# Performance work log

Hardware: AMD Instinct MI355X
Metric: run time of the kernel (lower is better)

The kernel has to match this reference:

```python
import jax, jax.numpy as jnp
import numpy as np

HEADS = 8
EPS = 1e-5

def setup_inputs() -> dict:
    key = jax.random.key(0)
    ks = jax.random.split(key, 4)
    B, S, N, C = 1, 256, 384, 512
    msa = jax.random.normal(ks[0], (B, S, N, C), dtype=jnp.float32)
    mask = jnp.ones((B, S), dtype=jnp.int32)
    Wqkv = jax.random.normal(ks[1], (3 * C, C), dtype=jnp.float32) * (C ** -0.5)
    bqkv = jnp.zeros((3 * C,), dtype=jnp.float32)
    Wout = jax.random.normal(ks[2], (C, C), dtype=jnp.float32) * (C ** -0.5)
    bout = jnp.zeros((C,), dtype=jnp.float32)
    gamma = jnp.ones((C,), dtype=jnp.float32)
    beta = jnp.zeros((C,), dtype=jnp.float32)
    return {"msa": msa, "mask": mask, "Wqkv": Wqkv, "bqkv": bqkv,
            "Wout": Wout, "bout": bout, "gamma": gamma, "beta": beta}

def reference(msa, mask, Wqkv, bqkv, Wout, bout, gamma, beta):
    B, S, N, C = msa.shape
    H = HEADS
    Dh = C // H
    scale = Dh ** -0.5
    msa_t = jnp.transpose(msa, (0, 2, 1, 3))            # [B,N,S,C]
    qkv = msa_t @ Wqkv.T + bqkv                          # [B,N,S,3C]
    qkv = qkv.reshape(B, N, S, 3, H, Dh)
    q, k, v = qkv[..., 0, :, :], qkv[..., 1, :, :], qkv[..., 2, :, :]  # [B,N,S,H,Dh]
    attn = jnp.einsum('bnshc,bnthc->bhst', q, k) * scale  # reduce over N and head-dim
    attn = jnp.where(mask[:, None, None, :] == 0, -1e9, attn)
    attn = jax.nn.softmax(attn, axis=-1)                 # [B,H,S,S]
    out = jnp.einsum('bhst,bnthc->bnshc', attn, v).reshape(B, N, S, C)
    out = jnp.transpose(out, (0, 2, 1, 3))               # [B,S,N,C]
    out = out @ Wout.T + bout
    x = msa + out
    mu = jnp.mean(x, axis=-1, keepdims=True)
    var = jnp.mean((x - mu) ** 2, axis=-1, keepdims=True)
    return (x - mu) * jax.lax.rsqrt(var + EPS) * gamma + beta
```

## Files before the change

### kernel.cpp

```cpp
#include <hip/hip_runtime.h>

#define S_ 256
#define N_ 384
#define C_ 512
#define H_ 8
#define R_ (N_*S_)
#define SPLITK 32
#define NPK (N_/SPLITK)

typedef _Float16 f16;
typedef _Float16 f16x8 __attribute__((ext_vector_type(8)));
typedef float f32x4 __attribute__((ext_vector_type(4)));

#define MFMA16(a,b,c) __builtin_amdgcn_mfma_f32_16x16x32_f16(a,b,c,0,0,0)

typedef __attribute__((address_space(3))) unsigned int as3_u32;
typedef __attribute__((address_space(1))) const unsigned int as1_u32;

__device__ __forceinline__ void gl_lds16(const void* g, void* l) {
    __builtin_amdgcn_global_load_lds((as1_u32*)(unsigned long long)g,
                                     (as3_u32*)(unsigned long long)l, 16, 0, 0);
}

__device__ __forceinline__ int swz_off(int row, int g) {
    return row*64 + (((g) ^ (row & 7)) << 3);
}

__device__ __forceinline__ void stage8(const f16* __restrict__ Ab,
                                       const f16* __restrict__ Bb,
                                       int stride, f16* As_, f16* Bs_,
                                       int tid, int wid) {
#pragma unroll
    for (int i = 0; i < 2; ++i) {
        int id = (i << 9) + tid;
        int row = id >> 3, g = (id & 7) ^ (row & 7);
        int lofs = ((i << 9) + (wid << 6)) << 4;
        gl_lds16(Ab + row * stride + (g << 3), (char*)As_ + lofs);
        gl_lds16(Bb + row * stride + (g << 3), (char*)Bs_ + lofs);
    }
}

__device__ __forceinline__ void mma8(const f16* As_, const f16* Bs_,
                                     int lane, int wr, int wc, f32x4 acc[4][2]) {
#pragma unroll
    for (int ks = 0; ks < 64; ks += 32) {
        int kg = (ks >> 3) + (lane >> 4);
        f16x8 af[4], bf[2];
#pragma unroll
        for (int m = 0; m < 4; ++m)
            af[m] = *(const f16x8*)&As_[swz_off(wr + (m << 4) + (lane & 15), kg)];
#pragma unroll
        for (int j = 0; j < 2; ++j)
            bf[j] = *(const f16x8*)&Bs_[swz_off(wc + (j << 4) + (lane & 15), kg)];
#pragma unroll
        for (int m = 0; m < 4; ++m)
#pragma unroll
            for (int j = 0; j < 2; ++j)
                acc[m][j] = MFMA16(af[m], bf[j], acc[m][j]);
    }
}

__device__ __forceinline__ void frag_mma64(const f16* As_, const f16* Bs_,
                                           int lane, int wr, int wc, f32x4 acc[4][4]) {
#pragma unroll
    for (int ks = 0; ks < 64; ks += 32) {
        int kg = (ks >> 3) + (lane >> 4);
        f16x8 af[4], bf[4];
#pragma unroll
        for (int m = 0; m < 4; ++m)
            af[m] = *(const f16x8*)&As_[swz_off(wr + (m << 4) + (lane & 15), kg)];
#pragma unroll
        for (int j = 0; j < 4; ++j)
            bf[j] = *(const f16x8*)&Bs_[swz_off(wc + (j << 4) + (lane & 15), kg)];
#pragma unroll
        for (int m = 0; m < 4; ++m)
#pragma unroll
            for (int j = 0; j < 4; ++j)
                acc[m][j] = MFMA16(af[m], bf[j], acc[m][j]);
    }
}

__global__ __launch_bounds__(256) void k_prep(const float* __restrict__ Wqkv,
                                              const float* __restrict__ Wout,
                                              f16* __restrict__ Wq16, f16* __restrict__ Wo16) {
    int i = blockIdx.x * 256 + threadIdx.x;
    if (i < 1536 * C_) Wq16[i] = (f16)Wqkv[i];
    if (i < C_ * C_)   Wo16[i] = (f16)Wout[i];
}

__global__ __launch_bounds__(256) void k_cast(const float* __restrict__ msa,
                                              f16* __restrict__ msaT) {
    int t = blockIdx.x * 256 + threadIdx.x;
    int r = t >> 6, cg = t & 63;
    int n = r >> 8, s = r & 255;
    const float* src = msa + (s * N_ + n) * C_ + (cg << 3);
    float4 lo = *(const float4*)src;
    float4 hi = *(const float4*)(src + 4);
    f16x8 v;
    v[0]=(f16)lo.x; v[1]=(f16)lo.y; v[2]=(f16)lo.z; v[3]=(f16)lo.w;
    v[4]=(f16)hi.x; v[5]=(f16)hi.y; v[6]=(f16)hi.z; v[7]=(f16)hi.w;
    *(f16x8*)(msaT + r * C_ + (cg << 3)) = v;
}

__global__ __launch_bounds__(512) void k_qkv(const f16* __restrict__ msaT,
                                             const f16* __restrict__ W,
                                             const float* __restrict__ bqkv,
                                             f16* __restrict__ qk,
                                             f16* __restrict__ vT) {
    int wg = (blockIdx.x & 7) * 1152 + (blockIdx.x >> 3);
    int bx = wg / 12, by = wg % 12;
    int j0 = by << 7;
    int tid = threadIdx.x, lane = tid & 63, wid = tid >> 6;
    int wr = (wid >> 2) << 6, wc = (wid & 3) << 5;
    __shared__ f16 SH[32768];
    const f16* Abase = msaT + (bx << 7) * C_;
    const f16* Bbase = W + j0 * C_;
    f32x4 acc[4][2] = {};
    stage8(Abase, Bbase, C_, SH, SH + 8192, tid, wid);
    __syncthreads();
    for (int kt = 0; kt < 8; ++kt) {
        int cur = kt & 1;
        if (kt < 7)
            stage8(Abase + ((kt + 1) << 6), Bbase + ((kt + 1) << 6), C_,
                   SH + ((cur ^ 1) << 14), SH + 8192 + ((cur ^ 1) << 14), tid, wid);
        mma8(SH + (cur << 14), SH + 8192 + (cur << 14), lane, wr, wc, acc);
        __syncthreads();
    }
    if (by < 8) {
#pragma unroll
        for (int m = 0; m < 4; ++m) {
            int rl = wr + (m << 4) + ((lane >> 4) << 2);
#pragma unroll
            for (int j = 0; j < 2; ++j) {
                int col = wc + (j << 4) + (lane & 15);
                float bv = bqkv[j0 + col];
#pragma unroll
                for (int q = 0; q < 4; ++q)
                    SH[(rl + q) * 140 + col] = (f16)(acc[m][j][q] + bv);
            }
        }
        __syncthreads();
#pragma unroll
        for (int i = 0; i < 4; ++i) {
            int u = (i << 9) + tid;
            int row = u >> 4, seg = u & 15;
            *(f16x8*)(qk + ((bx << 7) + row) * 1024 + j0 + (seg << 3)) =
                *(const f16x8*)&SH[row * 140 + (seg << 3)];
        }
    } else {
        int n = bx >> 1, t0g = (bx & 1) << 7;
#pragma unroll
        for (int m = 0; m < 4; ++m) {
            int rl = wr + (m << 4) + ((lane >> 4) << 2);
#pragma unroll
            for (int j = 0; j < 2; ++j) {
                int col = wc + (j << 4) + (lane & 15);
                float bv = bqkv[1024 + ((by - 8) << 7) + col];
#pragma unroll
                for (int q = 0; q < 4; ++q)
                    SH[col * 140 + rl + q] = (f16)(acc[m][j][q] + bv);
            }
        }
        __syncthreads();
#pragma unroll
        for (int i = 0; i < 4; ++i) {
            int u = (i << 9) + tid;
            int lcol = u >> 4, seg = u & 15;
            int jg = ((by - 8) << 7) + lcol;
            *(f16x8*)(vT + ((n * H_ + (jg >> 6)) * 64 + (jg & 63)) * S_ + t0g + (seg << 3)) =
                *(const f16x8*)&SH[lcol * 140 + (seg << 3)];
        }
    }
}

__global__ __launch_bounds__(512) void k_logits(const f16* __restrict__ qk,
                                                float* __restrict__ logP) {
    int wg = (blockIdx.x & 7) * 128 + (blockIdx.x >> 3);
    int sk = wg >> 5, rem = wg & 31, h = rem >> 2, sb = (rem >> 1) & 1, tb = rem & 1;
    int s0 = sb << 7, t0 = tb << 7, n0 = sk * NPK;
    int tid = threadIdx.x, lane = tid & 63, wid = tid >> 6;
    int wr = (wid >> 2) << 6, wc = (wid & 3) << 5;
    __shared__ f16 SH[32768];
    const f16* Aroot = qk + s0 * 1024 + (h << 6);
    const f16* Broot = qk + t0 * 1024 + 512 + (h << 6);
    f32x4 acc[4][2] = {};
    stage8(Aroot + n0 * S_ * 1024, Broot + n0 * S_ * 1024, 1024,
           SH, SH + 8192, tid, wid);
    __syncthreads();
    for (int t = 0; t < NPK; ++t) {
        int cur = t & 1;
        if (t < NPK - 1) {
            int n = n0 + t + 1;
            stage8(Aroot + n * S_ * 1024, Broot + n * S_ * 1024, 1024,
                   SH + ((cur ^ 1) << 14), SH + 8192 + ((cur ^ 1) << 14), tid, wid);
        }
        mma8(SH + (cur << 14), SH + 8192 + (cur << 14), lane, wr, wc, acc);
        __syncthreads();
    }
#pragma unroll
    for (int m = 0; m < 4; ++m) {
        int rl = wr + (m << 4) + ((lane >> 4) << 2);
#pragma unroll
        for (int j = 0; j < 2; ++j) {
            int tc = t0 + wc + (j << 4) + (lane & 15);
#pragma unroll
            for (int q = 0; q < 4; ++q)
                logP[((sk * H_ + h) * S_ + s0 + rl + q) * S_ + tc] = acc[m][j][q];
        }
    }
}

__global__ __launch_bounds__(256) void k_softmax(const float* __restrict__ logP,
                                                 const int* __restrict__ mask,
                                                 f16* __restrict__ attn) {
    int hs = blockIdx.x;
    int t = threadIdx.x, lane = t & 63, wid = t >> 6;
    float v = 0.f;
#pragma unroll
    for (int sk = 0; sk < SPLITK; ++sk)
        v += logP[(sk * H_ * S_ + hs) * S_ + t];
    v *= 0.125f;
    if (mask[t] == 0) v = -1e9f;
    __shared__ float redm[4], reds[4];
    float m_ = v;
    for (int o = 32; o > 0; o >>= 1) m_ = fmaxf(m_, __shfl_xor(m_, o));
    if (lane == 0) redm[wid] = m_;
    __syncthreads();
    float bm = fmaxf(fmaxf(redm[0], redm[1]), fmaxf(redm[2], redm[3]));
    float e = __expf(v - bm);
    float s_ = e;
    for (int o = 32; o > 0; o >>= 1) s_ += __shfl_xor(s_, o);
    if (lane == 0) reds[wid] = s_;
    __syncthreads();
    float tot = reds[0] + reds[1] + reds[2] + reds[3];
    attn[hs * S_ + t] = (f16)(e / tot);
}

__global__ __launch_bounds__(256) void k_pv(const f16* __restrict__ attn,
                                            const f16* __restrict__ vT,
                                            f16* __restrict__ attn_out) {
    int n = blockIdx.x >> 3, h = blockIdx.x & 7;
    int tid = threadIdx.x, lane = tid & 63, wid = tid >> 6;
    __shared__ f16 SH[20480];
    f16* As_ = SH;
    f16* Bs_ = SH + 16384;
    f32x4 acc[4][4] = {};
    const f16* Ab = attn + h * S_ * S_;
    const f16* Bb = vT + (n * H_ + h) * 64 * S_;
    for (int tt = 0; tt < 4; ++tt) {
        int t0 = tt << 6;
        __syncthreads();
#pragma unroll
        for (int i = 0; i < 8; ++i) {
            int id = (i << 8) + tid;
            int row = id >> 3, g = (id & 7) ^ (row & 7);
            int lofs = ((i << 8) + (wid << 6)) << 4;
            gl_lds16(Ab + row * S_ + t0 + (g << 3), (char*)As_ + lofs);
        }
#pragma unroll
        for (int i = 0; i < 2; ++i) {
            int id = (i << 8) + tid;
            int row = id >> 3, g = (id & 7) ^ (row & 7);
            int lofs = ((i << 8) + (wid << 6)) << 4;
            gl_lds16(Bb + row * S_ + t0 + (g << 3), (char*)Bs_ + lofs);
        }
        __syncthreads();
        frag_mma64(As_, Bs_, lane, wid << 6, 0, acc);
    }
#pragma unroll
    for (int p = 0; p < 2; ++p) {
        __syncthreads();
#pragma unroll
        for (int mm = 0; mm < 2; ++mm) {
            int m = 2 * p + mm;
            int rl = ((m & 1) << 4) + ((lane >> 4) << 2);
            int lrow = (wid << 5) + rl;
#pragma unroll
            for (int j = 0; j < 4; ++j) {
                int d = (j << 4) + (lane & 15);
#pragma unroll
                for (int q = 0; q < 4; ++q)
                    SH[(lrow + q) * 140 + d] = (f16)acc[m][j][q];
            }
        }
        __syncthreads();
#pragma unroll
        for (int i = 0; i < 4; ++i) {
            int u = tid + (i << 8);
            int row = u >> 3, seg = u & 7;
            int s = ((row >> 5) << 6) + (p << 5) + (row & 31);
            *(f16x8*)(attn_out + (n * S_ + s) * C_ + (h << 6) + (seg << 3)) =
                *(const f16x8*)&SH[row * 140 + (seg << 3)];
        }
    }
}

__global__ __launch_bounds__(512) void k_out_ln(const f16* __restrict__ attn_out,
                                                const f16* __restrict__ Wo,
                                                const float* __restrict__ bout,
                                                const f16* __restrict__ msaT,
                                                const float* __restrict__ gamma,
                                                const float* __restrict__ beta,
                                                float* __restrict__ out) {
    int r0 = blockIdx.x << 6;
    int n = r0 >> 8, s0 = r0 & 255;
    int tid = threadIdx.x, lane = tid & 63, wid = tid >> 6;
    __shared__ f16 SH[36864];
    f16* As_ = SH;
    f16* Bs_ = SH + 4096;
    __shared__ float redS[8][64], redQ[8][64], muS[64], rsS[64];
    f32x4 acc[4][4] = {};
    for (int kt = 0; kt < 8; ++kt) {
        int c0 = kt << 6;
        __syncthreads();
        {
            int row = tid >> 3, g = (tid & 7) ^ (row & 7);
            int lofs = (wid << 6) << 4;
            gl_lds16(attn_out + (r0 + row) * C_ + c0 + (g << 3), (char*)As_ + lofs);
        }
#pragma unroll
        for (int i = 0; i < 8; ++i) {
            int id = (i << 9) + tid;
            int row = id >> 3, g = (id & 7) ^ (row & 7);
            int lofs = ((i << 9) + (wid << 6)) << 4;
            gl_lds16(Wo + row * C_ + c0 + (g << 3), (char*)Bs_ + lofs);
        }
        __syncthreads();
        frag_mma64(As_, Bs_, lane, 0, wid << 6, acc);
    }
    float psum[4][4] = {}, psq[4][4] = {};
#pragma unroll
    for (int m = 0; m < 4; ++m)
#pragma unroll
        for (int j = 0; j < 4; ++j) {
            int c = (wid << 6) + (j << 4) + (lane & 15);
            float bj = bout[c];
#pragma unroll
            for (int q = 0; q < 4; ++q) {
                int rl = (m << 4) + ((lane >> 4) << 2) + q;
                float x = acc[m][j][q] + bj + (float)msaT[(r0 + rl) * C_ + c];
                acc[m][j][q] = x;
                psum[m][q] += x;
                psq[m][q] += x * x;
            }
        }
#pragma unroll
    for (int m = 0; m < 4; ++m)
#pragma unroll
        for (int q = 0; q < 4; ++q)
            for (int o = 1; o < 16; o <<= 1) {
                psum[m][q] += __shfl_xor(psum[m][q], o);
                psq[m][q]  += __shfl_xor(psq[m][q], o);
            }
    if ((lane & 15) == 0) {
#pragma unroll
        for (int m = 0; m < 4; ++m)
#pragma unroll
            for (int q = 0; q < 4; ++q) {
                int rl = (m << 4) + ((lane >> 4) << 2) + q;
                redS[wid][rl] = psum[m][q];
                redQ[wid][rl] = psq[m][q];
            }
    }
    __syncthreads();
    if (tid < 64) {
        float t1 = 0.f, t2 = 0.f;
#pragma unroll
        for (int w = 0; w < 8; ++w) { t1 += redS[w][tid]; t2 += redQ[w][tid]; }
        float mu = t1 * (1.0f / 512.0f);
        float var = t2 * (1.0f / 512.0f) - mu * mu;
        muS[tid] = mu;
        rsS[tid] = rsqrtf(var + 1e-5f);
    }
    __syncthreads();
#pragma unroll
    for (int m = 0; m < 4; ++m)
#pragma unroll
        for (int j = 0; j < 4; ++j) {
            int c = (wid << 6) + (j << 4) + (lane & 15);
            float g = gamma[c], bb = beta[c];
#pragma unroll
            for (int q = 0; q < 4; ++q) {
                int rl = (m << 4) + ((lane >> 4) << 2) + q;
                int s = s0 + rl;
                float y = (acc[m][j][q] - muS[rl]) * rsS[rl] * g + bb;
                out[(s * N_ + n) * C_ + c] = y;
            }
        }
}

extern "C" void kernel_launch(void* const* d_in, const int* in_sizes, int n_in,
                              void* d_out, int out_size, void* d_ws, size_t ws_size,
                              hipStream_t stream) {
    const float* msa   = (const float*)d_in[0];
    const int*   mask  = (const int*)d_in[1];
    const float* Wqkv  = (const float*)d_in[2];
    const float* bqkv  = (const float*)d_in[3];
    const float* Wout  = (const float*)d_in[4];
    const float* bout  = (const float*)d_in[5];
    const float* gamma = (const float*)d_in[6];
    const float* beta  = (const float*)d_in[7];
    float* out = (float*)d_out;
    char* ws = (char*)d_ws;

    f16*   qk   = (f16*)(ws);
    f16*   vT   = (f16*)(ws + 201326592);
    f16*   msaT = (f16*)(ws + 301989888);
    f16*   attn = (f16*)(ws + 402653184);
    f16*   Wq16 = (f16*)(ws + 403701760);
    f16*   Wo16 = (f16*)(ws + 405274624);
    float* logP = out;
    f16*   attn_out = qk;

    k_prep<<<dim3(3072), dim3(256), 0, stream>>>(Wqkv, Wout, Wq16, Wo16);
    k_cast<<<dim3(24576), dim3(256), 0, stream>>>(msa, msaT);
    k_qkv<<<dim3(9216), dim3(512), 0, stream>>>(msaT, Wq16, bqkv, qk, vT);
    k_logits<<<dim3(1024), dim3(512), 0, stream>>>(qk, logP);
    k_softmax<<<dim3(2048), dim3(256), 0, stream>>>(logP, mask, attn);
    k_pv<<<dim3(3072), dim3(256), 0, stream>>>(attn, vT, attn_out);
    k_out_ln<<<dim3(1536), dim3(512), 0, stream>>>(attn_out, Wo16, bout, msaT, gamma, beta, out);
}
```

Baseline: 580.2 us.

## Load B operands directly from global in PV and out-proj, fuse weight cast

```diff
diff --git a/kernel.cpp b/kernel.cpp
--- a/kernel.cpp
+++ b/kernel.cpp
@@ -60,37 +60,15 @@
     }
 }
 
-__device__ __forceinline__ void frag_mma64(const f16* As_, const f16* Bs_,
-                                           int lane, int wr, int wc, f32x4 acc[4][4]) {
-#pragma unroll
-    for (int ks = 0; ks < 64; ks += 32) {
-        int kg = (ks >> 3) + (lane >> 4);
-        f16x8 af[4], bf[4];
-#pragma unroll
-        for (int m = 0; m < 4; ++m)
-            af[m] = *(const f16x8*)&As_[swz_off(wr + (m << 4) + (lane & 15), kg)];
-#pragma unroll
-        for (int j = 0; j < 4; ++j)
-            bf[j] = *(const f16x8*)&Bs_[swz_off(wc + (j << 4) + (lane & 15), kg)];
-#pragma unroll
-        for (int m = 0; m < 4; ++m)
-#pragma unroll
-            for (int j = 0; j < 4; ++j)
-                acc[m][j] = MFMA16(af[m], bf[j], acc[m][j]);
-    }
-}
-
-__global__ __launch_bounds__(256) void k_prep(const float* __restrict__ Wqkv,
+__global__ __launch_bounds__(256) void k_cast(const float* __restrict__ msa,
+                                              const float* __restrict__ Wqkv,
                                               const float* __restrict__ Wout,
-                                              f16* __restrict__ Wq16, f16* __restrict__ Wo16) {
-    int i = blockIdx.x * 256 + threadIdx.x;
-    if (i < 1536 * C_) Wq16[i] = (f16)Wqkv[i];
-    if (i < C_ * C_)   Wo16[i] = (f16)Wout[i];
-}
-
-__global__ __launch_bounds__(256) void k_cast(const float* __restrict__ msa,
-                                              f16* __restrict__ msaT) {
+                                              f16* __restrict__ msaT,
+                                              f16* __restrict__ Wq16,
+                                              f16* __restrict__ Wo16) {
     int t = blockIdx.x * 256 + threadIdx.x;
+    if (t < 1536 * C_) Wq16[t] = (f16)Wqkv[t];
+    if (t < C_ * C_)   Wo16[t] = (f16)Wout[t];
     int r = t >> 6, cg = t & 63;
     int n = r >> 8, s = r & 255;
     const float* src = msa + (s * N_ + n) * C_ + (cg << 3);
@@ -106,7 +84,7 @@
                                              const f16* __restrict__ W,
                                              const float* __restrict__ bqkv,
                                              f16* __restrict__ qk,
-                                             f16* __restrict__ vT) {
+                                             f16* __restrict__ vB) {
     int wg = (blockIdx.x & 7) * 1152 + (blockIdx.x >> 3);
     int bx = wg / 12, by = wg % 12;
     int j0 = by << 7;
@@ -165,10 +143,12 @@
 #pragma unroll
         for (int i = 0; i < 4; ++i) {
             int u = (i << 9) + tid;
-            int lcol = u >> 4, seg = u & 15;
+            int c6 = u & 63, hh = (u >> 6) & 1, sg = u >> 7;
+            int lcol = (hh << 6) + c6;
             int jg = ((by - 8) << 7) + lcol;
-            *(f16x8*)(vT + ((n * H_ + (jg >> 6)) * 64 + (jg & 63)) * S_ + t0g + (seg << 3)) =
-                *(const f16x8*)&SH[lcol * 140 + (seg << 3)];
+            int h = jg >> 6;
+            *(f16x8*)(vB + (((n * H_ + h) << 5) + (t0g >> 3) + sg) * 512 + (c6 << 3)) =
+                *(const f16x8*)&SH[lcol * 140 + (sg << 3)];
         }
     }
 }
@@ -237,16 +217,15 @@
 }
 
 __global__ __launch_bounds__(256) void k_pv(const f16* __restrict__ attn,
-                                            const f16* __restrict__ vT,
+                                            const f16* __restrict__ vB,
                                             f16* __restrict__ attn_out) {
     int n = blockIdx.x >> 3, h = blockIdx.x & 7;
     int tid = threadIdx.x, lane = tid & 63, wid = tid >> 6;
-    __shared__ f16 SH[20480];
+    __shared__ f16 SH[17920];
     f16* As_ = SH;
-    f16* Bs_ = SH + 16384;
     f32x4 acc[4][4] = {};
     const f16* Ab = attn + h * S_ * S_;
-    const f16* Bb = vT + (n * H_ + h) * 64 * S_;
+    const f16* vBb = vB + ((n * H_ + h) << 5) * 512;
     for (int tt = 0; tt < 4; ++tt) {
         int t0 = tt << 6;
         __syncthreads();
@@ -257,15 +236,24 @@
             int lofs = ((i << 8) + (wid << 6)) << 4;
             gl_lds16(Ab + row * S_ + t0 + (g << 3), (char*)As_ + lofs);
         }
-#pragma unroll
-        for (int i = 0; i < 2; ++i) {
-            int id = (i << 8) + tid;
-            int row = id >> 3, g = (id & 7) ^ (row & 7);
-            int lofs = ((i << 8) + (wid << 6)) << 4;
-            gl_lds16(Bb + row * S_ + t0 + (g << 3), (char*)Bs_ + lofs);
-        }
-        __syncthreads();
-        frag_mma64(As_, Bs_, lane, wid << 6, 0, acc);
+        __syncthreads();
+#pragma unroll
+        for (int ks = 0; ks < 64; ks += 32) {
+            int kg = (ks >> 3) + (lane >> 4);
+            f16x8 af[4], bf[4];
+#pragma unroll
+            for (int m = 0; m < 4; ++m)
+                af[m] = *(const f16x8*)&As_[swz_off((wid << 6) + (m << 4) + (lane & 15), kg)];
+#pragma unroll
+            for (int j = 0; j < 4; ++j)
+                bf[j] = *(const f16x8*)(vBb + ((t0 >> 3) + kg) * 512 +
+                                        (((j << 4) + (lane & 15)) << 3));
+#pragma unroll
+            for (int m = 0; m < 4; ++m)
+#pragma unroll
+                for (int j = 0; j < 4; ++j)
+                    acc[m][j] = MFMA16(af[m], bf[j], acc[m][j]);
+        }
     }
 #pragma unroll
     for (int p = 0; p < 2; ++p) {
@@ -305,11 +293,10 @@
     int r0 = blockIdx.x << 6;
     int n = r0 >> 8, s0 = r0 & 255;
     int tid = threadIdx.x, lane = tid & 63, wid = tid >> 6;
-    __shared__ f16 SH[36864];
-    f16* As_ = SH;
-    f16* Bs_ = SH + 4096;
+    __shared__ f16 As_[4096];
     __shared__ float redS[8][64], redQ[8][64], muS[64], rsS[64];
     f32x4 acc[4][4] = {};
+    const f16* Wob = Wo + ((wid << 6) + (lane & 15)) * C_;
     for (int kt = 0; kt < 8; ++kt) {
         int c0 = kt << 6;
         __syncthreads();
@@ -318,15 +305,23 @@
             int lofs = (wid << 6) << 4;
             gl_lds16(attn_out + (r0 + row) * C_ + c0 + (g << 3), (char*)As_ + lofs);
         }
-#pragma unroll
-        for (int i = 0; i < 8; ++i) {
-            int id = (i << 9) + tid;
-            int row = id >> 3, g = (id & 7) ^ (row & 7);
-            int lofs = ((i << 9) + (wid << 6)) << 4;
-            gl_lds16(Wo + row * C_ + c0 + (g << 3), (char*)Bs_ + lofs);
-        }
-        __syncthreads();
-        frag_mma64(As_, Bs_, lane, 0, wid << 6, acc);
+        __syncthreads();
+#pragma unroll
+        for (int ks = 0; ks < 64; ks += 32) {
+            int kg = (ks >> 3) + (lane >> 4);
+            f16x8 af[4], bf[4];
+#pragma unroll
+            for (int m = 0; m < 4; ++m)
+                af[m] = *(const f16x8*)&As_[swz_off((m << 4) + (lane & 15), kg)];
+#pragma unroll
+            for (int j = 0; j < 4; ++j)
+                bf[j] = *(const f16x8*)(Wob + (j << 4) * C_ + c0 + (kg << 3));
+#pragma unroll
+            for (int m = 0; m < 4; ++m)
+#pragma unroll
+                for (int j = 0; j < 4; ++j)
+                    acc[m][j] = MFMA16(af[m], bf[j], acc[m][j]);
+        }
     }
     float psum[4][4] = {}, psq[4][4] = {};
 #pragma unroll
@@ -404,7 +399,7 @@
     char* ws = (char*)d_ws;
 
     f16*   qk   = (f16*)(ws);
-    f16*   vT   = (f16*)(ws + 201326592);
+    f16*   vB   = (f16*)(ws + 201326592);
     f16*   msaT = (f16*)(ws + 301989888);
     f16*   attn = (f16*)(ws + 402653184);
     f16*   Wq16 = (f16*)(ws + 403701760);
@@ -412,11 +407,10 @@
     float* logP = out;
     f16*   attn_out = qk;
 
-    k_prep<<<dim3(3072), dim3(256), 0, stream>>>(Wqkv, Wout, Wq16, Wo16);
-    k_cast<<<dim3(24576), dim3(256), 0, stream>>>(msa, msaT);
-    k_qkv<<<dim3(9216), dim3(512), 0, stream>>>(msaT, Wq16, bqkv, qk, vT);
+    k_cast<<<dim3(24576), dim3(256), 0, stream>>>(msa, Wqkv, Wout, msaT, Wq16, Wo16);
+    k_qkv<<<dim3(9216), dim3(512), 0, stream>>>(msaT, Wq16, bqkv, qk, vB);
     k_logits<<<dim3(1024), dim3(512), 0, stream>>>(qk, logP);
     k_softmax<<<dim3(2048), dim3(256), 0, stream>>>(logP, mask, attn);
-    k_pv<<<dim3(3072), dim3(256), 0, stream>>>(attn, vT, attn_out);
+    k_pv<<<dim3(3072), dim3(256), 0, stream>>>(attn, vB, attn_out);
     k_out_ln<<<dim3(1536), dim3(512), 0, stream>>>(attn_out, Wo16, bout, msaT, gamma, beta, out);
 }
```

Measured after the change: 619.9 us. 6.8% more time.

## Overlap next-tile loads with MFMA via partial vmcnt waits; fuse weight cast

Applied to the files above, without the earlier changes.

```diff
diff --git a/kernel.cpp b/kernel.cpp
--- a/kernel.cpp
+++ b/kernel.cpp
@@ -80,17 +80,15 @@
     }
 }
 
-__global__ __launch_bounds__(256) void k_prep(const float* __restrict__ Wqkv,
+__global__ __launch_bounds__(256) void k_cast(const float* __restrict__ msa,
+                                              const float* __restrict__ Wqkv,
                                               const float* __restrict__ Wout,
-                                              f16* __restrict__ Wq16, f16* __restrict__ Wo16) {
-    int i = blockIdx.x * 256 + threadIdx.x;
-    if (i < 1536 * C_) Wq16[i] = (f16)Wqkv[i];
-    if (i < C_ * C_)   Wo16[i] = (f16)Wout[i];
-}
-
-__global__ __launch_bounds__(256) void k_cast(const float* __restrict__ msa,
-                                              f16* __restrict__ msaT) {
+                                              f16* __restrict__ msaT,
+                                              f16* __restrict__ Wq16,
+                                              f16* __restrict__ Wo16) {
     int t = blockIdx.x * 256 + threadIdx.x;
+    if (t < 1536 * C_) Wq16[t] = (f16)Wqkv[t];
+    if (t < C_ * C_)   Wo16[t] = (f16)Wout[t];
     int r = t >> 6, cg = t & 63;
     int n = r >> 8, s = r & 255;
     const float* src = msa + (s * N_ + n) * C_ + (cg << 3);
@@ -117,14 +115,18 @@
     const f16* Bbase = W + j0 * C_;
     f32x4 acc[4][2] = {};
     stage8(Abase, Bbase, C_, SH, SH + 8192, tid, wid);
-    __syncthreads();
     for (int kt = 0; kt < 8; ++kt) {
         int cur = kt & 1;
-        if (kt < 7)
+        if (kt < 7) {
             stage8(Abase + ((kt + 1) << 6), Bbase + ((kt + 1) << 6), C_,
                    SH + ((cur ^ 1) << 14), SH + 8192 + ((cur ^ 1) << 14), tid, wid);
+            asm volatile("s_waitcnt vmcnt(4)" ::: "memory");
+        } else {
+            asm volatile("s_waitcnt vmcnt(0)" ::: "memory");
+        }
+        asm volatile("s_barrier" ::: "memory");
         mma8(SH + (cur << 14), SH + 8192 + (cur << 14), lane, wr, wc, acc);
-        __syncthreads();
+        asm volatile("s_barrier" ::: "memory");
     }
     if (by < 8) {
 #pragma unroll
@@ -186,16 +188,19 @@
     f32x4 acc[4][2] = {};
     stage8(Aroot + n0 * S_ * 1024, Broot + n0 * S_ * 1024, 1024,
            SH, SH + 8192, tid, wid);
-    __syncthreads();
     for (int t = 0; t < NPK; ++t) {
         int cur = t & 1;
         if (t < NPK - 1) {
             int n = n0 + t + 1;
             stage8(Aroot + n * S_ * 1024, Broot + n * S_ * 1024, 1024,
                    SH + ((cur ^ 1) << 14), SH + 8192 + ((cur ^ 1) << 14), tid, wid);
-        }
+            asm volatile("s_waitcnt vmcnt(4)" ::: "memory");
+        } else {
+            asm volatile("s_waitcnt vmcnt(0)" ::: "memory");
+        }
+        asm volatile("s_barrier" ::: "memory");
         mma8(SH + (cur << 14), SH + 8192 + (cur << 14), lane, wr, wc, acc);
-        __syncthreads();
+        asm volatile("s_barrier" ::: "memory");
     }
 #pragma unroll
     for (int m = 0; m < 4; ++m) {
@@ -412,8 +417,7 @@
     float* logP = out;
     f16*   attn_out = qk;
 
-    k_prep<<<dim3(3072), dim3(256), 0, stream>>>(Wqkv, Wout, Wq16, Wo16);
-    k_cast<<<dim3(24576), dim3(256), 0, stream>>>(msa, msaT);
+    k_cast<<<dim3(24576), dim3(256), 0, stream>>>(msa, Wqkv, Wout, msaT, Wq16, Wo16);
     k_qkv<<<dim3(9216), dim3(512), 0, stream>>>(msaT, Wq16, bqkv, qk, vT);
     k_logits<<<dim3(1024), dim3(512), 0, stream>>>(qk, logP);
     k_softmax<<<dim3(2048), dim3(256), 0, stream>>>(logP, mask, attn);
```

Measured after the change: 563.3 us. -2.9%, faster.
